# Performance work log

Measured on AMD Instinct MI355X. Metric: run time of the kernel, lower is better.

## Reference

```python
import jax, jax.numpy as jnp
import numpy as np

ACTION_IDS = jnp.array([7, 8, 9])
PREF_IDS = jnp.array([10, 11])
SPECIAL_IDS = jnp.array([0, 1, 2])  # <PAD>, <BOS>, <EOS>
NEG = -1e9


def setup_inputs() -> dict:
    key = jax.random.key(0)
    k1, k2 = jax.random.split(key)
    input_ids = jax.random.randint(k1, (1, 8192), 0, 16)
    emb_weight = jax.random.normal(k2, (16, 64), dtype=jnp.float32) * 0.02
    return {"input_ids": input_ids, "emb_weight": emb_weight}


def reference(input_ids, emb_weight):
    ids = input_ids[0]                      # [L]
    L = ids.shape[0]
    V = emb_weight.shape[0]

    # hidden states: plain embedding lookup
    h = emb_weight[input_ids]               # [1, L, 64]

    # ---- rule-based logits ----
    tok = jnp.arange(V)
    is_pref_tok = jnp.isin(tok, PREF_IDS)
    is_special_tok = jnp.isin(tok, SPECIAL_IDS)
    # row when previous token is an action: only pref tokens get 5.0
    row_action = jnp.where(is_pref_tok, 5.0, NEG)
    # row otherwise: 1.0 for non-special tokens, then pref tokens overwritten to -5.0
    row_other = jnp.where(is_pref_tok, -5.0, jnp.where(is_special_tok, NEG, 1.0))

    prev_is_action = jnp.isin(ids[:-1], ACTION_IDS)           # [L-1]
    next_logits = jnp.where(prev_is_action[:, None], row_action[None, :], row_other[None, :])  # [L-1, V]
    logits = jnp.concatenate([jnp.full((1, V), NEG, dtype=jnp.float32),
                              next_logits.astype(jnp.float32)], axis=0)[None]  # [1, L, V]

    # ---- rule-based attention ----
    i = jnp.arange(L)
    is_pref = jnp.isin(ids, PREF_IDS)                          # token i is a preference word
    prev_action = jnp.concatenate([jnp.zeros((1,), bool), jnp.isin(ids[:-1], ACTION_IDS)])
    cond = is_pref & (i > 0) & prev_action                     # rows with focused attention

    each = 0.2 / (L - 1)
    # focused row: 0.8 on column i-1, 0.2/(L-1) everywhere else
    special = jnp.where(i[None, :] == (i - 1)[:, None], 0.8, each)  # [L, L]
    attn = jnp.where(cond[:, None], special, 1.0 / L)[None, None]   # [1, 1, L, L]
    attn = attn.astype(jnp.float32)

    return logits, attn, h
```

## Files before the change

kernel.cpp:

```cpp
#include <hip/hip_runtime.h>
#include <hip/hip_bf16.h>


#define VOCAB 16
#define DIM 64
#define NEGV -1e9f

__global__ __launch_bounds__(256) void rulelm_fused(
    const int* __restrict__ ids,
    const float* __restrict__ emb,
    float* __restrict__ logits,
    float* __restrict__ attn,
    float* __restrict__ h,
    int L)
{
    const int i   = blockIdx.x;
    const int tid = threadIdx.x;

    const int id  = ids[i];
    const int idp = (i > 0) ? ids[i - 1] : -1;

    const bool prev_action = (i > 0) && (idp >= 7 && idp <= 9);
    const bool is_pref     = (id == 10) || (id == 11);
    const bool cond        = is_pref && prev_action;

    const float each = 0.2f / (float)(L - 1);
    const float base = cond ? each : (1.0f / (float)L);
    float4 fill = make_float4(base, base, base, base);

    float4* arow = (float4*)(attn + (size_t)i * (size_t)L);
    const int nvec = L >> 2;

    if (cond) {
        const int special = i - 1;
        for (int k = tid; k < nvec; k += 256) {
            float4 w = fill;
            const int c0 = k << 2;
            if (special >= c0 && special < c0 + 4) {
                ((float*)&w)[special - c0] = 0.8f;
            }
            arow[k] = w;
        }
    } else {
        for (int k = tid; k < nvec; k += 256) {
            arow[k] = fill;
        }
    }

    if (tid < VOCAB) {
        float val;
        const bool tok_pref = (tid == 10) || (tid == 11);
        if (i == 0) {
            val = NEGV;
        } else if (prev_action) {
            val = tok_pref ? 5.0f : NEGV;
        } else {
            val = tok_pref ? -5.0f : ((tid <= 2) ? NEGV : 1.0f);
        }
        logits[(size_t)i * VOCAB + tid] = val;
    }

    if (tid >= 64 && tid < 80) {
        const int q = tid - 64;
        ((float4*)(h + (size_t)i * DIM))[q] =
            ((const float4*)(emb + (size_t)id * DIM))[q];
    }
}

extern "C" void kernel_launch(void* const* d_in, const int* in_sizes, int n_in,
                              void* d_out, int out_size, void* d_ws, size_t ws_size,
                              hipStream_t stream)
{
    const int*   ids = (const int*)d_in[0];
    const float* emb = (const float*)d_in[1];
    const int L = in_sizes[0];

    float* out    = (float*)d_out;
    float* logits = out;
    float* attn   = out + (size_t)L * VOCAB;
    float* h      = attn + (size_t)L * (size_t)L;

    rulelm_fused<<<L, 256, 0, stream>>>(ids, emb, logits, attn, h, L);
}
```

Baseline: 47.44 us.

## Replace per-row blocks with flat grid-stride sweep over all outputs

Rewrites the kernel so a fixed grid of 2048 blocks sweeps the logits, hidden-state and attention outputs as flat float4 arrays instead of launching one block per row. The row index is derived with a shift and made wave-uniform with readfirstlane, and the row flags are recomputed per element. This aims to reduce block scheduling overhead and keep stores streaming evenly. In exchange it adds per-element ids loads and relies on L/4 being a power of two.

```diff
diff --git a/kernel.cpp b/kernel.cpp
--- a/kernel.cpp
+++ b/kernel.cpp
@@ -6,7 +6,9 @@
 #define DIM 64
 #define NEGV -1e9f
 
-__global__ __launch_bounds__(256) void rulelm_fused(
+typedef float f32x4 __attribute__((ext_vector_type(4)));
+
+__global__ __launch_bounds__(256) void rulelm_sweep(
     const int* __restrict__ ids,
     const float* __restrict__ emb,
     float* __restrict__ logits,
@@ -14,56 +16,59 @@
     float* __restrict__ h,
     int L)
 {
-    const int i   = blockIdx.x;
-    const int tid = threadIdx.x;
+    const int g        = blockIdx.x * 256 + threadIdx.x;
+    const int nthreads = gridDim.x * 256;
 
-    const int id  = ids[i];
-    const int idp = (i > 0) ? ids[i - 1] : -1;
+    const float invL = 1.0f / (float)L;
+    const float each = 0.2f / (float)(L - 1);
 
-    const bool prev_action = (i > 0) && (idp >= 7 && idp <= 9);
-    const bool is_pref     = (id == 10) || (id == 11);
-    const bool cond        = is_pref && prev_action;
-
-    const float each = 0.2f / (float)(L - 1);
-    const float base = cond ? each : (1.0f / (float)L);
-    float4 fill = make_float4(base, base, base, base);
-
-    float4* arow = (float4*)(attn + (size_t)i * (size_t)L);
-    const int nvec = L >> 2;
-
-    if (cond) {
-        const int special = i - 1;
-        for (int k = tid; k < nvec; k += 256) {
-            float4 w = fill;
-            const int c0 = k << 2;
-            if (special >= c0 && special < c0 + 4) {
-                ((float*)&w)[special - c0] = 0.8f;
-            }
-            arow[k] = w;
+    const int nlog = (L * VOCAB) >> 2;
+    for (int k = g; k < nlog; k += nthreads) {
+        const int row = k >> 2;
+        const int c0  = (k & 3) << 2;
+        const int idp = (row > 0) ? ids[row - 1] : -1;
+        const bool pa = (row > 0) && (idp >= 7 && idp <= 9);
+        f32x4 w;
+#pragma unroll
+        for (int j = 0; j < 4; ++j) {
+            const int tok = c0 + j;
+            const bool tp = (tok == 10) || (tok == 11);
+            float v;
+            if (row == 0)  v = NEGV;
+            else if (pa)   v = tp ? 5.0f : NEGV;
+            else           v = tp ? -5.0f : ((tok <= 2) ? NEGV : 1.0f);
+            w[j] = v;
         }
-    } else {
-        for (int k = tid; k < nvec; k += 256) {
-            arow[k] = fill;
-        }
+        ((f32x4*)logits)[k] = w;
     }
 
-    if (tid < VOCAB) {
-        float val;
-        const bool tok_pref = (tid == 10) || (tid == 11);
-        if (i == 0) {
-            val = NEGV;
-        } else if (prev_action) {
-            val = tok_pref ? 5.0f : NEGV;
-        } else {
-            val = tok_pref ? -5.0f : ((tid <= 2) ? NEGV : 1.0f);
-        }
-        logits[(size_t)i * VOCAB + tid] = val;
+    const int nh = (L * DIM) >> 2;
+    for (int k = g; k < nh; k += nthreads) {
+        const int row = k >> 4;
+        const int q   = k & 15;
+        ((f32x4*)h)[k] = ((const f32x4*)emb)[ids[row] * (DIM >> 2) + q];
     }
 
-    if (tid >= 64 && tid < 80) {
-        const int q = tid - 64;
-        ((float4*)(h + (size_t)i * DIM))[q] =
-            ((const float4*)(emb + (size_t)id * DIM))[q];
+    const int rsh = 31 - __builtin_clz(L >> 2);
+    const size_t nattn = ((size_t)L * (size_t)L) >> 2;
+    f32x4* __restrict__ ap = (f32x4*)attn;
+
+#pragma unroll 4
+    for (size_t k = g; k < nattn; k += (size_t)nthreads) {
+        const int row = __builtin_amdgcn_readfirstlane((int)(k >> rsh));
+        const int id  = ids[row];
+        const int idp = (row > 0) ? ids[row - 1] : -1;
+        const bool pa   = (row > 0) && (idp >= 7 && idp <= 9);
+        const bool cond = ((id == 10) || (id == 11)) && pa;
+        if (!cond) {
+            f32x4 w = {invL, invL, invL, invL};
+            ap[k] = w;
+        } else {
+            f32x4 w = {each, each, each, each};
+            const size_t ks = ((size_t)row << rsh) + (size_t)((row - 1) >> 2);
+            if (k == ks) w[(row - 1) & 3] = 0.8f;
+            ap[k] = w;
+        }
     }
 }
 
@@ -80,5 +85,5 @@
     float* attn   = out + (size_t)L * VOCAB;
     float* h      = attn + (size_t)L * (size_t)L;
 
-    rulelm_fused<<<L, 256, 0, stream>>>(ids, emb, logits, attn, h, L);
+    rulelm_sweep<<<2048, 256, 0, stream>>>(ids, emb, logits, attn, h, L);
 }
```

After: 47.17 us. No clear change (-0.6%).
